# Performance work log

Measured on AMD Instinct MI355X. Metric: run time of the kernel, lower is better.

The kernel has to match this reference:

```python
import jax, jax.numpy as jnp
import numpy as np

HIDDEN = 4096
N_HEADS = 32
N_KV = 32
HEAD_DIM = HIDDEN // N_HEADS  # 128
T = 2048
THETA = 10000.0
EPS = 1e-5


def setup_inputs() -> dict:
    key = jax.random.key(0)
    ks = jax.random.split(key, 7)
    s = 0.02
    return {
        "positions": jnp.arange(T, dtype=jnp.int64),
        "hidden_states": jax.random.normal(ks[0], (T, HIDDEN), jnp.float32),
        "w_qkv": jax.random.normal(ks[1], ((N_HEADS + 2 * N_KV) * HEAD_DIM, HIDDEN), jnp.float32) * s,
        "w_o": jax.random.normal(ks[2], (HIDDEN, N_HEADS * HEAD_DIM), jnp.float32) * s,
        "q_norm_w": jnp.ones((N_HEADS, HEAD_DIM), jnp.float32) + jax.random.normal(ks[3], (N_HEADS, HEAD_DIM), jnp.float32) * s,
        "q_norm_b": jax.random.normal(ks[4], (N_HEADS, HEAD_DIM), jnp.float32) * s,
        "k_norm_w": jnp.ones((N_KV, HEAD_DIM), jnp.float32) + jax.random.normal(ks[5], (N_KV, HEAD_DIM), jnp.float32) * s,
        "k_norm_b": jax.random.normal(ks[6], (N_KV, HEAD_DIM), jnp.float32) * s,
    }


def _layer_norm_affine(x, w, b):
    # x: [T, H, d]; normalize over last dim, no affine inside, then per-head affine
    mu = jnp.mean(x, axis=-1, keepdims=True)
    var = jnp.var(x, axis=-1, keepdims=True)
    xn = (x - mu) * jax.lax.rsqrt(var + EPS)
    return xn * w + b


def _rope_neox(x, positions):
    # x: [T, H, d], NEOX style: rotate halves over full head_dim
    half = HEAD_DIM // 2
    inv_freq = 1.0 / (THETA ** (jnp.arange(0, half, dtype=jnp.float32) * 2.0 / HEAD_DIM))
    ang = positions.astype(jnp.float32)[:, None] * inv_freq  # [T, half]
    cos = jnp.cos(ang)[:, None, :]
    sin = jnp.sin(ang)[:, None, :]
    x1, x2 = x[..., :half], x[..., half:]
    return jnp.concatenate([x1 * cos - x2 * sin, x2 * cos + x1 * sin], axis=-1)


def reference(positions, hidden_states, w_qkv, w_o, q_norm_w, q_norm_b, k_norm_w, k_norm_b):
    qkv = hidden_states @ w_qkv.T  # [T, (H+2Hkv)*d]
    q_size = N_HEADS * HEAD_DIM
    kv_size = N_KV * HEAD_DIM
    q = qkv[:, :q_size].reshape(T, N_HEADS, HEAD_DIM)
    k = qkv[:, q_size:q_size + kv_size].reshape(T, N_KV, HEAD_DIM)
    v = qkv[:, q_size + kv_size:].reshape(T, N_KV, HEAD_DIM)

    q = _layer_norm_affine(q, q_norm_w, q_norm_b)
    k = _layer_norm_affine(k, k_norm_w, k_norm_b)
    q = _rope_neox(q, positions)
    k = _rope_neox(k, positions)

    scale = HEAD_DIM ** -0.5
    scores = jnp.einsum('thd,shd->hts', q, k) * scale  # [H, T, T]
    causal = jnp.tril(jnp.ones((T, T), dtype=bool))
    scores = jnp.where(causal[None], scores, jnp.finfo(scores.dtype).min)
    p = jax.nn.softmax(scores, axis=-1)
    attn = jnp.einsum('hts,shd->thd', p, v).reshape(T, N_HEADS * HEAD_DIM)
    return attn @ w_o.T
```

## Files before the change

kernel.cpp:

```cpp
#include <hip/hip_runtime.h>
#include <cstdint>

#define T_SEQ 2048
#define HID   4096
#define NH    32
#define HD    128
#define QKVW  12288

typedef float  f32x4  __attribute__((ext_vector_type(4)));
typedef __bf16 bf16x8 __attribute__((ext_vector_type(8)));

#define QSCALE (0.08838834764831845f * 1.4426950408889634f)

__device__ __forceinline__ unsigned short f2bf(float f) {
  unsigned int u = __builtin_bit_cast(unsigned int, f);
  u += 0x7fffu + ((u >> 16) & 1u);
  return (unsigned short)(u >> 16);
}
__device__ __forceinline__ float bf2f(unsigned short u) {
  return __builtin_bit_cast(float, (unsigned int)u << 16);
}

__device__ __forceinline__ void gload_lds16(const void* gptr, void* lptr) {
  __builtin_amdgcn_global_load_lds(
      (const __attribute__((address_space(1))) unsigned int*)(unsigned long long)(uintptr_t)gptr,
      (__attribute__((address_space(3))) unsigned int*)(unsigned int)(uintptr_t)lptr,
      16, 0, 0);
}

#define SB __builtin_amdgcn_sched_barrier(0)

__device__ __forceinline__ void cvt_store8(void* lds, float4 v) {
  unsigned int lo, hi;
  asm("v_cvt_pk_bf16_f32 %0, %1, %2" : "=v"(lo) : "v"(v.x), "v"(v.y));
  asm("v_cvt_pk_bf16_f32 %0, %1, %2" : "=v"(hi) : "v"(v.z), "v"(v.w));
  uint2 p; p.x = lo; p.y = hi;
  *(uint2*)lds = p;
}

__global__ __launch_bounds__(256) void cast_bf16(const float* __restrict__ in,
                                                 unsigned short* __restrict__ out,
                                                 int n4) {
  int i = blockIdx.x * 256 + threadIdx.x;
  int stride = gridDim.x * 256;
  for (; i < n4; i += stride) {
    float4 v = ((const float4*)in)[i];
    ushort4 o;
    o.x = f2bf(v.x); o.y = f2bf(v.y); o.z = f2bf(v.z); o.w = f2bf(v.w);
    ((ushort4*)out)[i] = o;
  }
}

__global__ __launch_bounds__(512, 2) void gemm_bt8(const unsigned short* __restrict__ Ag,
                                                   const float* __restrict__ Bg,
                                                   unsigned short* __restrict__ C,
                                                   int M, int N, int K, int MT) {
  __shared__ unsigned short As_[2][256 * 64];
  __shared__ unsigned short Bs_[2][192 * 64];
  const int tid  = threadIdx.x;
  const int lane = tid & 63;
  const int w    = tid >> 6;
  const int wm   = w & 3;
  const int wn   = w >> 2;
  const int l15  = lane & 15;
  const int lg   = lane >> 4;
  const int sw   = l15 & 7;

  const int cpx = gridDim.x >> 3;
  const int swz = (blockIdx.x & 7) * cpx + (blockIdx.x >> 3);
  const int bm  = (swz % MT) * 256;
  const int bn  = (swz / MT) * 192;
  const int nk  = K >> 6;

  const unsigned short* Abase = Ag + (size_t)bm * K;
  const float*          Bbase = Bg + (size_t)bn * K;

  int bofs[6], blds[6];
#pragma unroll
  for (int j = 0; j < 6; ++j) {
    const int hid = j * 512 + tid;
    const int cid = hid >> 1, hh = hid & 1;
    const int r = cid >> 3, ch = cid & 7;
    bofs[j] = r * K + ((ch ^ (r & 7)) * 8 + hh * 4);
    blds[j] = cid * 16 + hh * 8;
  }
  float4 btmp[6];

#define AST(buf, kt_) do {                                                      \
    _Pragma("unroll")                                                           \
    for (int _u = 0; _u < 4; ++_u) {                                            \
      const int _cid = _u * 512 + tid;                                          \
      const int _r = _cid >> 3, _ch = _cid & 7;                                 \
      gload_lds16(Abase + (size_t)_r * K + (size_t)(kt_) * 64 +                 \
                      ((_ch ^ (_r & 7)) * 8),                                   \
                  (void*)((char*)(buf) + _cid * 16));                           \
    } } while (0)
#define BLOAD(kt_) do {                                                         \
    _Pragma("unroll")                                                           \
    for (int _j = 0; _j < 6; ++_j)                                              \
      btmp[_j] = *(const float4*)(Bbase + (size_t)(kt_) * 64 + bofs[_j]);       \
  } while (0)
#define BSTORE(buf) do {                                                        \
    _Pragma("unroll")                                                           \
    for (int _j = 0; _j < 6; ++_j)                                              \
      cvt_store8((char*)(buf) + blds[_j], btmp[_j]);                            \
  } while (0)

#define RD(base, r, kk)                                                          \
  (*(const bf16x8*)((const char*)(base) + (r) * 128 + ((((kk) * 4 + lg) ^ sw) * 16)))

#define MFMA24(afr, bfr) do {                                                    \
    _Pragma("unroll")                                                            \
    for (int _m = 0; _m < 4; ++_m)                                               \
      _Pragma("unroll")                                                          \
      for (int _n = 0; _n < 6; ++_n)                                             \
        acc[_m][_n] = __builtin_amdgcn_mfma_f32_16x16x32_bf16(                   \
            afr[_m], bfr[_n], acc[_m][_n], 0, 0, 0);                             \
  } while (0)

  f32x4 acc[4][6] = {};

  BLOAD(0); SB;
  AST(As_[0], 0); SB;
  asm volatile("s_waitcnt vmcnt(4)" ::: "memory");
  SB;
  BSTORE(Bs_[0]); SB;
  BLOAD(1); SB;
  AST(As_[1], 1); SB;
  asm volatile("s_waitcnt vmcnt(10)" ::: "memory");
  asm volatile("s_waitcnt lgkmcnt(0)" ::: "memory");
  SB;
  __builtin_amdgcn_s_barrier();

  for (int t = 0; t < nk; ++t) {
    const int cur = t & 1;
    const unsigned short* As = As_[cur];
    const unsigned short* Bs = Bs_[cur];
    bf16x8 a0[4], a1[4], b0[6], b1[6];

    if (t + 1 < nk) { BSTORE(Bs_[cur ^ 1]); SB; }

#pragma unroll
    for (int m = 0; m < 4; ++m) a0[m] = RD(As, wm * 64 + m * 16 + l15, 0);
#pragma unroll
    for (int n = 0; n < 6; ++n) b0[n] = RD(Bs, wn * 96 + n * 16 + l15, 0);
    SB;
#pragma unroll
    for (int m = 0; m < 4; ++m) a1[m] = RD(As, wm * 64 + m * 16 + l15, 1);
#pragma unroll
    for (int n = 0; n < 6; ++n) b1[n] = RD(Bs, wn * 96 + n * 16 + l15, 1);
    SB;
    asm volatile("s_waitcnt lgkmcnt(10)" ::: "memory");
    SB;
    __builtin_amdgcn_s_setprio(1);
    MFMA24(a0, b0);
    __builtin_amdgcn_s_setprio(0);
    SB;
    asm volatile("s_waitcnt lgkmcnt(0)" ::: "memory");
    SB;
    __builtin_amdgcn_s_barrier();
    if (t + 2 < nk) { BLOAD(t + 2); SB; AST(As_[cur], t + 2); SB; }
    __builtin_amdgcn_s_setprio(1);
    MFMA24(a1, b1);
    __builtin_amdgcn_s_setprio(0);
    if (t + 1 < nk) {
      if (t + 2 < nk) asm volatile("s_waitcnt vmcnt(10)" ::: "memory");
      else            asm volatile("s_waitcnt vmcnt(0)" ::: "memory");
      SB;
      __builtin_amdgcn_s_barrier();
    }
  }
#undef AST
#undef BLOAD
#undef BSTORE
#undef RD
#undef MFMA24

#pragma unroll
  for (int m = 0; m < 4; ++m)
#pragma unroll
    for (int i = 0; i < 4; ++i) {
      const int row = bm + wm * 64 + m * 16 + lg * 4 + i;
#pragma unroll
      for (int n = 0; n < 6; ++n)
        C[(size_t)row * N + bn + wn * 96 + n * 16 + l15] = f2bf(acc[m][n][i]);
    }
}

__global__ __launch_bounds__(512, 2) void gemm2_bt8(const unsigned short* __restrict__ Ag,
                                                    const float* __restrict__ Bg,
                                                    float* __restrict__ C,
                                                    int M, int N, int K, int MT) {
  __shared__ unsigned short As_[2][256 * 64];
  __shared__ unsigned short Bs_[2][128 * 64];
  const int tid  = threadIdx.x;
  const int lane = tid & 63;
  const int w    = tid >> 6;
  const int wm   = w & 3;
  const int wn   = w >> 2;
  const int l15  = lane & 15;
  const int lg   = lane >> 4;
  const int sw   = l15 & 7;

  const int cpx = gridDim.x >> 3;
  const int swz = (blockIdx.x & 7) * cpx + (blockIdx.x >> 3);
  const int bm  = (swz % MT) * 256;
  const int bn  = (swz / MT) * 128;
  const int nk  = K >> 6;

  const unsigned short* Abase = Ag + (size_t)bm * K;
  const float*          Bbase = Bg + (size_t)bn * K;

  int bofs[4], blds[4];
#pragma unroll
  for (int j = 0; j < 4; ++j) {
    const int hid = j * 512 + tid;
    const int cid = hid >> 1, hh = hid & 1;
    const int r = cid >> 3, ch = cid & 7;
    bofs[j] = r * K + ((ch ^ (r & 7)) * 8 + hh * 4);
    blds[j] = cid * 16 + hh * 8;
  }
  float4 btmp[4];

#define AST(buf, kt_) do {                                                      \
    _Pragma("unroll")                                                           \
    for (int _u = 0; _u < 4; ++_u) {                                            \
      const int _cid = _u * 512 + tid;                                          \
      const int _r = _cid >> 3, _ch = _cid & 7;                                 \
      gload_lds16(Abase + (size_t)_r * K + (size_t)(kt_) * 64 +                 \
                      ((_ch ^ (_r & 7)) * 8),                                   \
                  (void*)((char*)(buf) + _cid * 16));                           \
    } } while (0)
#define BLOAD(kt_) do {                                                         \
    _Pragma("unroll")                                                           \
    for (int _j = 0; _j < 4; ++_j)                                              \
      btmp[_j] = *(const float4*)(Bbase + (size_t)(kt_) * 64 + bofs[_j]);       \
  } while (0)
#define BSTORE(buf) do {                                                        \
    _Pragma("unroll")                                                           \
    for (int _j = 0; _j < 4; ++_j)                                              \
      cvt_store8((char*)(buf) + blds[_j], btmp[_j]);                            \
  } while (0)

#define RD(base, r, kk)                                                          \
  (*(const bf16x8*)((const char*)(base) + (r) * 128 + ((((kk) * 4 + lg) ^ sw) * 16)))

#define MFMA16(afr, bfr) do {                                                    \
    _Pragma("unroll")                                                            \
    for (int _m = 0; _m < 4; ++_m)                                               \
      _Pragma("unroll")                                                          \
      for (int _n = 0; _n < 4; ++_n)                                             \
        acc[_m][_n] = __builtin_amdgcn_mfma_f32_16x16x32_bf16(                   \
            afr[_m], bfr[_n], acc[_m][_n], 0, 0, 0);                             \
  } while (0)

  f32x4 acc[4][4] = {};

  BLOAD(0); SB;
  AST(As_[0], 0); SB;
  asm volatile("s_waitcnt vmcnt(4)" ::: "memory");
  SB;
  BSTORE(Bs_[0]); SB;
  BLOAD(1); SB;
  AST(As_[1], 1); SB;
  asm volatile("s_waitcnt vmcnt(8)" ::: "memory");
  asm volatile("s_waitcnt lgkmcnt(0)" ::: "memory");
  SB;
  __builtin_amdgcn_s_barrier();

  for (int t = 0; t < nk; ++t) {
    const int cur = t & 1;
    const unsigned short* As = As_[cur];
    const unsigned short* Bs = Bs_[cur];
    bf16x8 a0[4], a1[4], b0[4], b1[4];

    if (t + 1 < nk) { BSTORE(Bs_[cur ^ 1]); SB; }

#pragma unroll
    for (int m = 0; m < 4; ++m) a0[m] = RD(As, wm * 64 + m * 16 + l15, 0);
#pragma unroll
    for (int n = 0; n < 4; ++n) b0[n] = RD(Bs, wn * 64 + n * 16 + l15, 0);
    SB;
#pragma unroll
    for (int m = 0; m < 4; ++m) a1[m] = RD(As, wm * 64 + m * 16 + l15, 1);
#pragma unroll
    for (int n = 0; n < 4; ++n) b1[n] = RD(Bs, wn * 64 + n * 16 + l15, 1);
    SB;
    asm volatile("s_waitcnt lgkmcnt(8)" ::: "memory");
    SB;
    __builtin_amdgcn_s_setprio(1);
    MFMA16(a0, b0);
    __builtin_amdgcn_s_setprio(0);
    SB;
    asm volatile("s_waitcnt lgkmcnt(0)" ::: "memory");
    SB;
    __builtin_amdgcn_s_barrier();
    if (t + 2 < nk) { BLOAD(t + 2); SB; AST(As_[cur], t + 2); SB; }
    __builtin_amdgcn_s_setprio(1);
    MFMA16(a1, b1);
    __builtin_amdgcn_s_setprio(0);
    if (t + 1 < nk) {
      if (t + 2 < nk) asm volatile("s_waitcnt vmcnt(8)" ::: "memory");
      else            asm volatile("s_waitcnt vmcnt(0)" ::: "memory");
      SB;
      __builtin_amdgcn_s_barrier();
    }
  }
#undef AST
#undef BLOAD
#undef BSTORE
#undef RD
#undef MFMA16

#pragma unroll
  for (int m = 0; m < 4; ++m)
#pragma unroll
    for (int i = 0; i < 4; ++i) {
      const int row = bm + wm * 64 + m * 16 + lg * 4 + i;
#pragma unroll
      for (int n = 0; n < 4; ++n)
        C[(size_t)row * N + bn + wn * 64 + n * 16 + l15] = acc[m][n][i];
    }
}

__global__ __launch_bounds__(256) void norm_rope(const unsigned short* __restrict__ qkv,
                                                 const float* __restrict__ qw,
                                                 const float* __restrict__ qb,
                                                 const float* __restrict__ kw,
                                                 const float* __restrict__ kb,
                                                 unsigned short* __restrict__ q,
                                                 unsigned short* __restrict__ k) {
  const int t    = blockIdx.x;
  const int tid  = threadIdx.x;
  const int lane = tid & 63;
  const int w    = tid >> 6;
  const float invf = exp2f(-(float)lane * (13.287712379549449f / 64.0f));
  const float ang  = (float)t * invf;
  const float c = cosf(ang), s = sinf(ang);
  const unsigned short* row = qkv + (size_t)t * QKVW;

#pragma unroll 1
  for (int sel = 0; sel < 2; ++sel) {
    const unsigned short* src = row + sel * HID;
    const float* wgt = sel ? kw : qw;
    const float* bia = sel ? kb : qb;
    unsigned short* dst = sel ? k : q;
    const float oscale = sel ? 1.0f : QSCALE;
    for (int h = w; h < NH; h += 4) {
      const unsigned short* x = src + h * HD;
      float x1 = bf2f(x[lane]), x2 = bf2f(x[lane + 64]);
      float sum = x1 + x2, ss = x1 * x1 + x2 * x2;
#pragma unroll
      for (int m = 1; m < 64; m <<= 1) {
        sum += __shfl_xor(sum, m, 64);
        ss  += __shfl_xor(ss, m, 64);
      }
      const float mu  = sum * (1.0f / 128.0f);
      const float var = ss * (1.0f / 128.0f) - mu * mu;
      const float r   = rsqrtf(var + 1e-5f);
      const float n1  = (x1 - mu) * r * wgt[h * HD + lane]      + bia[h * HD + lane];
      const float n2  = (x2 - mu) * r * wgt[h * HD + lane + 64] + bia[h * HD + lane + 64];
      const float o1  = (n1 * c - n2 * s) * oscale;
      const float o2  = (n2 * c + n1 * s) * oscale;
      dst[(size_t)t * HID + h * HD + lane]      = f2bf(o1);
      dst[(size_t)t * HID + h * HD + lane + 64] = f2bf(o2);
    }
  }
}

__global__ __launch_bounds__(256) void transpose_v(const unsigned short* __restrict__ v,
                                                   unsigned short* __restrict__ vt) {
  __shared__ unsigned short tile[64][65];
  const int h  = blockIdx.z;
  const int tt = blockIdx.x * 64;
  const int dd = blockIdx.y * 64;
  const int tid = threadIdx.x;
#pragma unroll
  for (int p = 0; p < 4; ++p) {
    int idx = p * 256 + tid;
    int r = idx >> 4, c4 = idx & 15;
    ushort4 val = *(const ushort4*)&v[(size_t)(tt + r) * QKVW + h * HD + dd + c4 * 4];
    tile[r][c4 * 4 + 0] = val.x;
    tile[r][c4 * 4 + 1] = val.y;
    tile[r][c4 * 4 + 2] = val.z;
    tile[r][c4 * 4 + 3] = val.w;
  }
  __syncthreads();
#pragma unroll
  for (int p = 0; p < 4; ++p) {
    int idx = p * 256 + tid;
    int r = idx >> 4, c4 = idx & 15;
    ushort4 o;
    o.x = tile[c4 * 4 + 0][r];
    o.y = tile[c4 * 4 + 1][r];
    o.z = tile[c4 * 4 + 2][r];
    o.w = tile[c4 * 4 + 3][r];
    *(ushort4*)&vt[((size_t)h * HD + dd + r) * T_SEQ + tt + c4 * 4] = o;
  }
}

__global__ __launch_bounds__(256) void attn_fwd(const unsigned short* __restrict__ Q,
                                                const unsigned short* __restrict__ K,
                                                const unsigned short* __restrict__ VT,
                                                unsigned short* __restrict__ O) {
  __shared__ unsigned short Ks[2][64 * 128];
  __shared__ unsigned short Vs[2][128 * 64];
  __shared__ unsigned short Ps[4][16 * 64];
  const int h    = blockIdx.y;
  const int pair = blockIdx.x;
  const int tid  = threadIdx.x;
  const int lane = tid & 63;
  const int w    = tid >> 6;
  const int l15  = lane & 15;
  const int lg   = lane >> 4;
  const int sw   = l15 & 7;

#pragma unroll 1
  for (int half = 0; half < 2; ++half) {
    const int qt   = half ? (31 - pair) : pair;
    const int qrow = qt * 64 + w * 16;

    bf16x8 qf[4];
#pragma unroll
    for (int kk = 0; kk < 4; ++kk)
      qf[kk] = *(const bf16x8*)&Q[(size_t)(qrow + l15) * HID + h * HD + kk * 32 + lg * 8];

    f32x4 o[8] = {};
    float mrow[4], lrow[4];
#pragma unroll
    for (int i = 0; i < 4; ++i) { mrow[i] = -1e30f; lrow[i] = 0.0f; }

    const int nkt = qt + 1;

    {
#pragma unroll
      for (int p = 0; p < 4; ++p) {
        const int c  = p * 256 + tid;
        const int kr = c >> 4, kc = c & 15;
        gload_lds16(&K[(size_t)kr * HID + h * HD + ((kc ^ (kr & 7)) * 8)],
                    &Ks[0][(p * 256 + w * 64) * 8]);
        const int vr = c >> 3, vc = c & 7;
        gload_lds16(&VT[((size_t)h * HD + vr) * T_SEQ + ((vc ^ (vr & 7)) * 8)],
                    &Vs[0][(p * 256 + w * 64) * 8]);
      }
    }
    __syncthreads();

#pragma unroll 1
    for (int kt = 0; kt < nkt; ++kt) {
      const int cur = kt & 1;
      if (kt + 1 < nkt) {
        const int k0 = (kt + 1) * 64;
#pragma unroll
        for (int p = 0; p < 4; ++p) {
          const int c  = p * 256 + tid;
          const int kr = c >> 4, kc = c & 15;
          gload_lds16(&K[(size_t)(k0 + kr) * HID + h * HD + ((kc ^ (kr & 7)) * 8)],
                      &Ks[cur ^ 1][(p * 256 + w * 64) * 8]);
          const int vr = c >> 3, vc = c & 7;
          gload_lds16(&VT[((size_t)h * HD + vr) * T_SEQ + k0 + ((vc ^ (vr & 7)) * 8)],
                      &Vs[cur ^ 1][(p * 256 + w * 64) * 8]);
        }
      }
      const unsigned short* ksb = Ks[cur];
      const unsigned short* vsb = Vs[cur];

      f32x4 sfr[4] = {};
#pragma unroll
      for (int n = 0; n < 4; ++n)
#pragma unroll
        for (int kk = 0; kk < 4; ++kk) {
          bf16x8 kf = *(const bf16x8*)&ksb[(n * 16 + l15) * 128 + ((kk * 4 + lg) ^ sw) * 8];
          sfr[n] = __builtin_amdgcn_mfma_f32_16x16x32_bf16(qf[kk], kf, sfr[n], 0, 0, 0);
        }

      if (kt == qt) {
#pragma unroll
        for (int n = 0; n < 4; ++n)
#pragma unroll
          for (int i = 0; i < 4; ++i)
            if (n * 16 + l15 > w * 16 + lg * 4 + i) sfr[n][i] = -1e30f;
      }

      float escale[4];
#pragma unroll
      for (int i = 0; i < 4; ++i) {
        float mx = fmaxf(fmaxf(sfr[0][i], sfr[1][i]), fmaxf(sfr[2][i], sfr[3][i]));
        mx = fmaxf(mx, __shfl_xor(mx, 1, 64));
        mx = fmaxf(mx, __shfl_xor(mx, 2, 64));
        mx = fmaxf(mx, __shfl_xor(mx, 4, 64));
        mx = fmaxf(mx, __shfl_xor(mx, 8, 64));
        const float mnew = fmaxf(mrow[i], mx);
        escale[i] = exp2f(mrow[i] - mnew);
        mrow[i] = mnew;
        const int prow = lg * 4 + i;
        float rs = 0.0f;
#pragma unroll
        for (int n = 0; n < 4; ++n) {
          const float p = exp2f(sfr[n][i] - mnew);
          rs += p;
          Ps[w][prow * 64 + (((2 * n + (l15 >> 3)) ^ (prow & 7)) * 8) + sw] = f2bf(p);
        }
        rs += __shfl_xor(rs, 1, 64);
        rs += __shfl_xor(rs, 2, 64);
        rs += __shfl_xor(rs, 4, 64);
        rs += __shfl_xor(rs, 8, 64);
        lrow[i] = lrow[i] * escale[i] + rs;
      }
#pragma unroll
      for (int f = 0; f < 8; ++f)
#pragma unroll
        for (int i = 0; i < 4; ++i) o[f][i] *= escale[i];

      asm volatile("s_waitcnt lgkmcnt(0)" ::: "memory");
      __builtin_amdgcn_sched_barrier(0);

      bf16x8 pf[2];
#pragma unroll
      for (int kk = 0; kk < 2; ++kk)
        pf[kk] = *(const bf16x8*)&Ps[w][l15 * 64 + ((kk * 4 + lg) ^ sw) * 8];
#pragma unroll
      for (int f = 0; f < 8; ++f)
#pragma unroll
        for (int kk = 0; kk < 2; ++kk) {
          bf16x8 vf = *(const bf16x8*)&vsb[(f * 16 + l15) * 64 + ((kk * 4 + lg) ^ sw) * 8];
          o[f] = __builtin_amdgcn_mfma_f32_16x16x32_bf16(pf[kk], vf, o[f], 0, 0, 0);
        }

      __syncthreads();
    }

#pragma unroll
    for (int i = 0; i < 4; ++i) {
      const float inv = 1.0f / lrow[i];
      const int trow = qrow + lg * 4 + i;
#pragma unroll
      for (int f = 0; f < 8; ++f)
        O[(size_t)trow * HID + h * HD + f * 16 + l15] = f2bf(o[f][i] * inv);
    }
  }
}

extern "C" void kernel_launch(void* const* d_in, const int* in_sizes, int n_in,
                              void* d_out, int out_size, void* d_ws, size_t ws_size,
                              hipStream_t stream) {
  const float* hidden = (const float*)d_in[1];
  const float* w_qkv  = (const float*)d_in[2];
  const float* w_o    = (const float*)d_in[3];
  const float* qw     = (const float*)d_in[4];
  const float* qb     = (const float*)d_in[5];
  const float* kw     = (const float*)d_in[6];
  const float* kb     = (const float*)d_in[7];

  char* ws = (char*)d_ws;
  unsigned short* attn_bf = (unsigned short*)(ws + 0);
  unsigned short* hid_bf  = (unsigned short*)(ws + 16777216);
  unsigned short* vt_bf   = (unsigned short*)(ws + 33554432);
  unsigned short* qkv_bf  = (unsigned short*)(ws + 50331648);
  unsigned short* q_bf    = (unsigned short*)(ws + 100663296);
  unsigned short* k_bf    = (unsigned short*)(ws + 117440512);

  cast_bf16<<<2048, 256, 0, stream>>>(hidden, hid_bf, (T_SEQ * HID) / 4);
  gemm_bt8<<<512, 512, 0, stream>>>(hid_bf, w_qkv, qkv_bf, T_SEQ, QKVW, HID, 8);
  norm_rope<<<T_SEQ, 256, 0, stream>>>(qkv_bf, qw, qb, kw, kb, q_bf, k_bf);
  transpose_v<<<dim3(T_SEQ / 64, HD / 64, NH), 256, 0, stream>>>(qkv_bf + 2 * HID, vt_bf);
  attn_fwd<<<dim3(16, NH), 256, 0, stream>>>(q_bf, k_bf, vt_bf, attn_bf);
  gemm2_bt8<<<256, 512, 0, stream>>>(attn_bf, w_o, (float*)d_out, T_SEQ, HID, HID, 8);
}
```

Measured before the change: 508.3 us.

## Pre-cast w_o to bf16 and stream both GEMM2 operands via direct-to-LDS loads

```diff
diff --git a/kernel.cpp b/kernel.cpp
--- a/kernel.cpp
+++ b/kernel.cpp
@@ -138,8 +138,6 @@
     const unsigned short* Bs = Bs_[cur];
     bf16x8 a0[4], a1[4], b0[6], b1[6];
 
-    if (t + 1 < nk) { BSTORE(Bs_[cur ^ 1]); SB; }
-
 #pragma unroll
     for (int m = 0; m < 4; ++m) a0[m] = RD(As, wm * 64 + m * 16 + l15, 0);
 #pragma unroll
@@ -159,6 +157,7 @@
     asm volatile("s_waitcnt lgkmcnt(0)" ::: "memory");
     SB;
     __builtin_amdgcn_s_barrier();
+    if (t + 1 < nk) { BSTORE(Bs_[cur ^ 1]); SB; }
     if (t + 2 < nk) { BLOAD(t + 2); SB; AST(As_[cur], t + 2); SB; }
     __builtin_amdgcn_s_setprio(1);
     MFMA24(a1, b1);
@@ -166,6 +165,7 @@
     if (t + 1 < nk) {
       if (t + 2 < nk) asm volatile("s_waitcnt vmcnt(10)" ::: "memory");
       else            asm volatile("s_waitcnt vmcnt(0)" ::: "memory");
+      asm volatile("s_waitcnt lgkmcnt(0)" ::: "memory");
       SB;
       __builtin_amdgcn_s_barrier();
     }
@@ -188,7 +188,7 @@
 }
 
 __global__ __launch_bounds__(512, 2) void gemm2_bt8(const unsigned short* __restrict__ Ag,
-                                                    const float* __restrict__ Bg,
+                                                    const unsigned short* __restrict__ Bg,
                                                     float* __restrict__ C,
                                                     int M, int N, int K, int MT) {
   __shared__ unsigned short As_[2][256 * 64];
@@ -209,37 +209,19 @@
   const int nk  = K >> 6;
 
   const unsigned short* Abase = Ag + (size_t)bm * K;
-  const float*          Bbase = Bg + (size_t)bn * K;
-
-  int bofs[4], blds[4];
-#pragma unroll
-  for (int j = 0; j < 4; ++j) {
-    const int hid = j * 512 + tid;
-    const int cid = hid >> 1, hh = hid & 1;
-    const int r = cid >> 3, ch = cid & 7;
-    bofs[j] = r * K + ((ch ^ (r & 7)) * 8 + hh * 4);
-    blds[j] = cid * 16 + hh * 8;
-  }
-  float4 btmp[4];
-
-#define AST(buf, kt_) do {                                                      \
-    _Pragma("unroll")                                                           \
-    for (int _u = 0; _u < 4; ++_u) {                                            \
-      const int _cid = _u * 512 + tid;                                          \
-      const int _r = _cid >> 3, _ch = _cid & 7;                                 \
-      gload_lds16(Abase + (size_t)_r * K + (size_t)(kt_) * 64 +                 \
-                      ((_ch ^ (_r & 7)) * 8),                                   \
-                  (void*)((char*)(buf) + _cid * 16));                           \
-    } } while (0)
-#define BLOAD(kt_) do {                                                         \
-    _Pragma("unroll")                                                           \
-    for (int _j = 0; _j < 4; ++_j)                                              \
-      btmp[_j] = *(const float4*)(Bbase + (size_t)(kt_) * 64 + bofs[_j]);       \
+  const unsigned short* Bbase = Bg + (size_t)bn * K;
+
+#define SG(ldsbase, gbase, kt_, u_) do {                                        \
+    const int _cid = (u_) * 512 + tid;                                          \
+    const int _r = _cid >> 3, _ch = _cid & 7;                                   \
+    gload_lds16((gbase) + (size_t)_r * K + (size_t)(kt_) * 64 +                 \
+                    ((_ch ^ (_r & 7)) * 8),                                     \
+                (void*)((char*)(ldsbase) + _cid * 16));                         \
   } while (0)
-#define BSTORE(buf) do {                                                        \
-    _Pragma("unroll")                                                           \
-    for (int _j = 0; _j < 4; ++_j)                                              \
-      cvt_store8((char*)(buf) + blds[_j], btmp[_j]);                            \
+#define STAGE(abuf, bbuf, kt_) do {                                             \
+    SG(abuf, Abase, kt_, 0); SG(abuf, Abase, kt_, 1);                           \
+    SG(abuf, Abase, kt_, 2); SG(abuf, Abase, kt_, 3);                           \
+    SG(bbuf, Bbase, kt_, 0); SG(bbuf, Bbase, kt_, 1);                           \
   } while (0)
 
 #define RD(base, r, kk)                                                          \
@@ -256,15 +238,13 @@
 
   f32x4 acc[4][4] = {};
 
-  BLOAD(0); SB;
-  AST(As_[0], 0); SB;
-  asm volatile("s_waitcnt vmcnt(4)" ::: "memory");
-  SB;
-  BSTORE(Bs_[0]); SB;
-  BLOAD(1); SB;
-  AST(As_[1], 1); SB;
-  asm volatile("s_waitcnt vmcnt(8)" ::: "memory");
-  asm volatile("s_waitcnt lgkmcnt(0)" ::: "memory");
+  STAGE(As_[0], Bs_[0], 0);
+  if (nk > 1) {
+    STAGE(As_[1], Bs_[1], 1);
+    asm volatile("s_waitcnt vmcnt(6)" ::: "memory");
+  } else {
+    asm volatile("s_waitcnt vmcnt(0)" ::: "memory");
+  }
   SB;
   __builtin_amdgcn_s_barrier();
 
@@ -274,8 +254,6 @@
     const unsigned short* Bs = Bs_[cur];
     bf16x8 a0[4], a1[4], b0[4], b1[4];
 
-    if (t + 1 < nk) { BSTORE(Bs_[cur ^ 1]); SB; }
-
 #pragma unroll
     for (int m = 0; m < 4; ++m) a0[m] = RD(As, wm * 64 + m * 16 + l15, 0);
 #pragma unroll
@@ -295,20 +273,20 @@
     asm volatile("s_waitcnt lgkmcnt(0)" ::: "memory");
     SB;
     __builtin_amdgcn_s_barrier();
-    if (t + 2 < nk) { BLOAD(t + 2); SB; AST(As_[cur], t + 2); SB; }
+    if (t + 2 < nk) STAGE(As_[cur], Bs_[cur], t + 2);
+    SB;
     __builtin_amdgcn_s_setprio(1);
     MFMA16(a1, b1);
     __builtin_amdgcn_s_setprio(0);
     if (t + 1 < nk) {
-      if (t + 2 < nk) asm volatile("s_waitcnt vmcnt(8)" ::: "memory");
+      if (t + 2 < nk) asm volatile("s_waitcnt vmcnt(6)" ::: "memory");
       else            asm volatile("s_waitcnt vmcnt(0)" ::: "memory");
       SB;
       __builtin_amdgcn_s_barrier();
     }
   }
-#undef AST
-#undef BLOAD
-#undef BSTORE
+#undef SG
+#undef STAGE
 #undef RD
 #undef MFMA16
 
@@ -554,16 +532,18 @@
 
   char* ws = (char*)d_ws;
   unsigned short* attn_bf = (unsigned short*)(ws + 0);
-  unsigned short* hid_bf  = (unsigned short*)(ws + 16777216);
-  unsigned short* vt_bf   = (unsigned short*)(ws + 33554432);
-  unsigned short* qkv_bf  = (unsigned short*)(ws + 50331648);
-  unsigned short* q_bf    = (unsigned short*)(ws + 100663296);
-  unsigned short* k_bf    = (unsigned short*)(ws + 117440512);
+  unsigned short* wo_bf   = (unsigned short*)(ws + 16777216);
+  unsigned short* hid_bf  = (unsigned short*)(ws + 50331648);
+  unsigned short* vt_bf   = (unsigned short*)(ws + 67108864);
+  unsigned short* qkv_bf  = (unsigned short*)(ws + 83886080);
+  unsigned short* q_bf    = (unsigned short*)(ws + 134217728);
+  unsigned short* k_bf    = (unsigned short*)(ws + 150994944);
 
   cast_bf16<<<2048, 256, 0, stream>>>(hidden, hid_bf, (T_SEQ * HID) / 4);
   gemm_bt8<<<512, 512, 0, stream>>>(hid_bf, w_qkv, qkv_bf, T_SEQ, QKVW, HID, 8);
+  cast_bf16<<<2048, 256, 0, stream>>>(w_o, wo_bf, (HID * HID) / 4);
   norm_rope<<<T_SEQ, 256, 0, stream>>>(qkv_bf, qw, qb, kw, kb, q_bf, k_bf);
   transpose_v<<<dim3(T_SEQ / 64, HD / 64, NH), 256, 0, stream>>>(qkv_bf + 2 * HID, vt_bf);
   attn_fwd<<<dim3(16, NH), 256, 0, stream>>>(q_bf, k_bf, vt_bf, attn_bf);
-  gemm2_bt8<<<256, 512, 0, stream>>>(attn_bf, w_o, (float*)d_out, T_SEQ, HID, HID, 8);
-}
+  gemm2_bt8<<<256, 512, 0, stream>>>(attn_bf, wo_bf, (float*)d_out, T_SEQ, HID, HID, 8);
+}
```

Result: faster. 475.1 us (-6.5%).
